# Kernel optimization log

Measured on AMD Instinct MI355X. Metric: run time of the kernel, lower is better.

## Reference

```python
import jax, jax.numpy as jnp
import numpy as np

NUM_USERS = 100000
NUM_ITEMS = 50000
N_NODES = NUM_USERS + NUM_ITEMS
EMB = 64
N_EDGES = 2000000
NUM_LAYERS = 3


def setup_inputs() -> dict:
    key = jax.random.key(0)
    ks = jax.random.split(key, 16)
    inp = {
        "edge_index": jax.random.randint(ks[0], (2, N_EDGES), 0, N_NODES, dtype=jnp.int64 if jax.config.jax_enable_x64 else jnp.int32),
        "user_features": jax.random.normal(ks[1], (NUM_USERS, 15), dtype=jnp.float32),
        "user_color_indices": jax.random.randint(ks[2], (NUM_USERS,), 0, 22),
        "user_size_indices": jax.random.randint(ks[3], (NUM_USERS,), 0, 18),
        "item_features": jax.random.normal(ks[4], (NUM_ITEMS, 17), dtype=jnp.float32),
        "user_emb_w": jax.random.normal(ks[5], (NUM_USERS, EMB), dtype=jnp.float32) * 0.01,
        "item_emb_w": jax.random.normal(ks[6], (NUM_ITEMS, EMB), dtype=jnp.float32) * 0.01,
        "user_numeric_W": jax.random.normal(ks[7], (EMB, 12), dtype=jnp.float32) * 0.1,
        "user_numeric_b": jnp.zeros((EMB,), dtype=jnp.float32),
        "user_vector_W": jax.random.normal(ks[8], (EMB, 3), dtype=jnp.float32) * 0.1,
        "user_vector_b": jnp.zeros((EMB,), dtype=jnp.float32),
        "color_emb_w": jax.random.normal(ks[9], (22, EMB), dtype=jnp.float32) * 0.1,
        "size_emb_w": jax.random.normal(ks[10], (18, EMB), dtype=jnp.float32) * 0.1,
        "item_numeric_W": jax.random.normal(ks[11], (EMB, 5), dtype=jnp.float32) * 0.1,
        "item_numeric_b": jnp.zeros((EMB,), dtype=jnp.float32),
        "item_vector_W": jax.random.normal(ks[12], (EMB, 12), dtype=jnp.float32) * 0.1,
        "item_vector_b": jnp.zeros((EMB,), dtype=jnp.float32),
    }
    return inp


def _lightgcn_conv(x, row, col, norm):
    # gather x at source (row), scale by per-edge norm, scatter-add at target (col)
    msg = norm[:, None] * x[row]                      # [E, d]
    return jax.ops.segment_sum(msg, col, num_segments=N_NODES)


def reference(edge_index, user_features, user_color_indices, user_size_indices,
              item_features, user_emb_w, item_emb_w,
              user_numeric_W, user_numeric_b, user_vector_W, user_vector_b,
              color_emb_w, size_emb_w,
              item_numeric_W, item_numeric_b, item_vector_W, item_vector_b):
    # multimodal feature fusion
    user_emb = (user_emb_w
                + user_features[:, :12] @ user_numeric_W.T + user_numeric_b
                + user_features[:, 12:15] @ user_vector_W.T + user_vector_b
                + color_emb_w[user_color_indices]
                + size_emb_w[user_size_indices])
    item_emb = (item_emb_w
                + item_features[:, :5] @ item_numeric_W.T + item_numeric_b
                + item_features[:, 5:] @ item_vector_W.T + item_vector_b)
    x = jnp.concatenate([user_emb, item_emb], axis=0)  # [N, d]

    row, col = edge_index[0], edge_index[1]
    # symmetric-normalization coefficients (degree over targets, as in source)
    deg = jax.ops.segment_sum(jnp.ones_like(col, dtype=x.dtype), col, num_segments=N_NODES)
    deg_inv_sqrt = jnp.where(deg > 0, jax.lax.rsqrt(jnp.maximum(deg, 1.0)), 0.0)
    norm = deg_inv_sqrt[row] * deg_inv_sqrt[col]       # [E]

    acc = x
    total = x
    for _ in range(NUM_LAYERS):
        acc = _lightgcn_conv(acc, row, col, norm)      # dropout in eval mode = identity
        total = total + acc
    final = total / (NUM_LAYERS + 1)

    return final[:NUM_USERS], final[NUM_USERS:]
```

## Files before the change

### kernel.cpp

```cpp
#include <hip/hip_runtime.h>

#define EMB 64
#define NBMAX 512
#define BCAP 8192
#define BSTRIDE 12288
#define CHUNK 4096


__device__ __forceinline__ unsigned short f2bf(float f) {
    union { float f; unsigned u; } c; c.f = f;
    unsigned r = c.u + 0x7fffu + ((c.u >> 16) & 1u);
    return (unsigned short)(r >> 16);
}
__device__ __forceinline__ float bflo(unsigned u) {
    union { unsigned u; float f; } c; c.u = u << 16; return c.f;
}
__device__ __forceinline__ float bfhi(unsigned u) {
    union { unsigned u; float f; } c; c.u = u & 0xffff0000u; return c.f;
}


__global__ void init_kernel(unsigned* __restrict__ p, int nz,
                            unsigned* __restrict__ dummyA,
                            unsigned* __restrict__ dummyB) {
    int i = blockIdx.x * blockDim.x + threadIdx.x;
    if (i < nz) p[i] = 0u;
    if (blockIdx.x == 0) {
        int t = threadIdx.x;
        if (t < 32) dummyA[t] = 0u;
        else if (t < 64) dummyB[t - 32] = 0u;
    }
}


__global__ void fuse_users_kernel(const float* __restrict__ feat,
                                  const int* __restrict__ cidx,
                                  const int* __restrict__ sidx,
                                  const float* __restrict__ emb_w,
                                  const float* __restrict__ Wn,
                                  const float* __restrict__ bn,
                                  const float* __restrict__ Wv,
                                  const float* __restrict__ bv,
                                  const float* __restrict__ color_w,
                                  const float* __restrict__ size_w,
                                  const float* __restrict__ dis,
                                  float* __restrict__ total,
                                  unsigned short* __restrict__ y0,
                                  int U) {
    int t = blockIdx.x * blockDim.x + threadIdx.x;
    int u = t >> 6, d = t & 63;
    if (u >= U) return;
    const float* f = feat + (size_t)u * 15;
    float acc = emb_w[(size_t)u * EMB + d] + bn[d] + bv[d];
#pragma unroll
    for (int k = 0; k < 12; ++k) acc = fmaf(f[k], Wn[d * 12 + k], acc);
#pragma unroll
    for (int k = 0; k < 3; ++k) acc = fmaf(f[12 + k], Wv[d * 3 + k], acc);
    acc += color_w[(size_t)cidx[u] * EMB + d];
    acc += size_w[(size_t)sidx[u] * EMB + d];
    size_t o = (size_t)u * EMB + d;
    total[o] = acc;
    y0[o] = f2bf(acc * dis[u]);
}

__global__ void fuse_items_kernel(const float* __restrict__ feat,
                                  const float* __restrict__ emb_w,
                                  const float* __restrict__ Wn,
                                  const float* __restrict__ bn,
                                  const float* __restrict__ Wv,
                                  const float* __restrict__ bv,
                                  const float* __restrict__ dis,
                                  float* __restrict__ total,
                                  unsigned short* __restrict__ y0,
                                  int I, int U) {
    int t = blockIdx.x * blockDim.x + threadIdx.x;
    int i = t >> 6, d = t & 63;
    if (i >= I) return;
    const float* f = feat + (size_t)i * 17;
    float acc = emb_w[(size_t)i * EMB + d] + bn[d] + bv[d];
#pragma unroll
    for (int k = 0; k < 5; ++k) acc = fmaf(f[k], Wn[d * 5 + k], acc);
#pragma unroll
    for (int k = 0; k < 12; ++k) acc = fmaf(f[5 + k], Wv[d * 12 + k], acc);
    int n = U + i;
    size_t o = (size_t)n * EMB + d;
    total[o] = acc;
    y0[o] = f2bf(acc * dis[n]);
}


__global__ __launch_bounds__(256) void partition_kernel(
        const int* __restrict__ row, const int* __restrict__ col,
        unsigned* __restrict__ bcursor, unsigned* __restrict__ bucketbuf,
        int E, int NB) {
    __shared__ unsigned h[NBMAX];
    __shared__ unsigned wbase[NBMAX];
    const int t = threadIdx.x;
    const long chunk = (long)blockIdx.x * CHUNK;

    for (int i = t; i < NB; i += 256) h[i] = 0u;
    __syncthreads();
    for (int it = 0; it < CHUNK / 256; ++it) {
        long e = chunk + (long)it * 256 + t;
        if (e < E) atomicAdd(&h[((unsigned)col[e]) >> 9], 1u);
    }
    __syncthreads();
    for (int i = t; i < NB; i += 256) {
        unsigned c = h[i];
        wbase[i] = c ? atomicAdd(&bcursor[i], c) : 0u;
    }
    __syncthreads();
    for (int i = t; i < NB; i += 256) h[i] = 0u;
    __syncthreads();
    for (int it = 0; it < CHUNK / 256; ++it) {
        long e = chunk + (long)it * 256 + t;
        if (e < E) {
            unsigned c = (unsigned)col[e];
            unsigned b = c >> 9;
            unsigned lpos = atomicAdd(&h[b], 1u);
            unsigned pos = wbase[b] + lpos;
            if (pos < BCAP)
                bucketbuf[(size_t)b * BCAP + pos] = (((unsigned)row[e]) << 9) | (c & 511u);
        }
    }
}


__global__ __launch_bounds__(256) void bucket_csr_kernel(
        const unsigned* __restrict__ bcursor,
        const unsigned* __restrict__ bucketbuf,
        uint4* __restrict__ meta,
        float* __restrict__ dis, unsigned* __restrict__ srcidx,
        unsigned* __restrict__ clsCnt,
        int N, int NB) {
    const int b = blockIdx.x;
    const int t = threadIdx.x;
    __shared__ unsigned hist[512];
    __shared__ unsigned ps[256];
    __shared__ unsigned cls[64];

    const unsigned base = (unsigned)b * BSTRIDE;
    unsigned cntb = bcursor[b];
    if (cntb > BCAP) cntb = BCAP;

    hist[2 * t] = 0u; hist[2 * t + 1] = 0u;
    if (t < 64) cls[t] = 0u;
    __syncthreads();
    const unsigned* buf = bucketbuf + (size_t)b * BCAP;
    for (unsigned j = t; j < cntb; j += 256) atomicAdd(&hist[buf[j] & 511u], 1u);
    __syncthreads();

    unsigned h0 = hist[2 * t], h1 = hist[2 * t + 1];
    unsigned c0p = (h0 + 7u) & ~7u, c1p = (h1 + 7u) & ~7u;
    ps[t] = c0p + c1p;
    __syncthreads();
    for (int off = 1; off < 256; off <<= 1) {
        unsigned y = (t >= off) ? ps[t - off] : 0u;
        __syncthreads();
        ps[t] += y;
        __syncthreads();
    }
    unsigned pexcl = ps[t] - (c0p + c1p);
    unsigned beg0 = base + pexcl, beg1 = beg0 + c0p;

    int n0 = (b << 9) + 2 * t, n1 = n0 + 1;
    if (n0 < N) {
        float dv = h0 ? rsqrtf((float)h0) : 0.f;
        meta[n0] = make_uint4(beg0, beg0 + c0p, __float_as_uint(dv), 0u);
        dis[n0] = dv;
        atomicAdd(&cls[min(c0p >> 3, 63u)], 1u);
        for (unsigned k = h0; k < c0p; ++k) srcidx[beg0 + k] = ((unsigned)N) << 5;
    }
    if (n1 < N) {
        float dv = h1 ? rsqrtf((float)h1) : 0.f;
        meta[n1] = make_uint4(beg1, beg1 + c1p, __float_as_uint(dv), 0u);
        dis[n1] = dv;
        atomicAdd(&cls[min(c1p >> 3, 63u)], 1u);
        for (unsigned k = h1; k < c1p; ++k) srcidx[beg1 + k] = ((unsigned)N) << 5;
    }
    __syncthreads();

    if (t < 64 && cls[t]) atomicAdd(&clsCnt[t], cls[t]);
    hist[2 * t] = beg0; hist[2 * t + 1] = beg1;
    __syncthreads();
    for (unsigned j = t; j < cntb; j += 256) {
        unsigned p = buf[j];
        unsigned pos = atomicAdd(&hist[p & 511u], 1u);
        srcidx[pos] = (p >> 9) << 5;
    }
}


__global__ void cls_scan_kernel(const unsigned* __restrict__ clsCnt,
                                unsigned* __restrict__ clsBase) {
    __shared__ unsigned sh[64];
    int t = threadIdx.x;
    if (t < 64) sh[t] = clsCnt[t];
    __syncthreads();
    if (t == 0) {
        unsigned run = 0;
        for (int i = 0; i < 64; ++i) { unsigned v = sh[i]; sh[i] = run; run += v; }
    }
    __syncthreads();
    if (t < 64) clsBase[t] = sh[t];
}


__global__ __launch_bounds__(256) void order_fill_kernel(
        const uint4* __restrict__ meta,
        const unsigned* __restrict__ clsBase, unsigned* __restrict__ clsCur,
        unsigned* __restrict__ order, int N) {
    __shared__ unsigned h[64], wb[64];
    int t = threadIdx.x;
    int n = blockIdx.x * 256 + t;
    if (t < 64) h[t] = 0u;
    __syncthreads();
    unsigned c = 0, lpos = 0;
    bool valid = n < N;
    if (valid) {
        uint4 md = meta[n];
        c = min((md.y - md.x) >> 3, 63u);
        lpos = atomicAdd(&h[c], 1u);
    }
    __syncthreads();
    if (t < 64) wb[t] = h[t] ? atomicAdd(&clsCur[t], h[t]) : 0u;
    __syncthreads();
    if (valid) order[clsBase[c] + wb[c] + lpos] = (unsigned)n;
}


__global__ __launch_bounds__(256) void gather_propagate_kernel(
        const unsigned* __restrict__ order, const uint4* __restrict__ meta,
        const unsigned* __restrict__ src,
        const unsigned* __restrict__ srcidx,
        unsigned* __restrict__ ynext,
        float4* __restrict__ total4,
        float scale, int N, int store) {
    int lane = threadIdx.x & 63;
    int slot = blockIdx.x * 8 + ((threadIdx.x >> 6) << 1) + (lane >> 5);
    bool active = slot < N;
    int n = active ? (int)order[slot] : 0;
    uint4 md = active ? meta[n] : make_uint4(0u, 0u, 0u, 0u);
    unsigned beg = md.x, endp = md.y;
    float dn = __uint_as_float(md.z);
    unsigned q = (unsigned)((lane >> 4) & 1);
    unsigned m2 = (unsigned)(lane & 15) * 2u;
    float s0 = 0.f, s1 = 0.f, s2 = 0.f, s3 = 0.f;
    for (unsigned j = beg; j < endp; j += 8) {
        uint4 iv = *reinterpret_cast<const uint4*>(&srcidx[j + 4u * q]);
        uint2 ua = *reinterpret_cast<const uint2*>(&src[iv.x + m2]);
        uint2 ub = *reinterpret_cast<const uint2*>(&src[iv.y + m2]);
        uint2 uc = *reinterpret_cast<const uint2*>(&src[iv.z + m2]);
        uint2 ud = *reinterpret_cast<const uint2*>(&src[iv.w + m2]);
        s0 += (bflo(ua.x) + bflo(ub.x)) + (bflo(uc.x) + bflo(ud.x));
        s1 += (bfhi(ua.x) + bfhi(ub.x)) + (bfhi(uc.x) + bfhi(ud.x));
        s2 += (bflo(ua.y) + bflo(ub.y)) + (bflo(uc.y) + bflo(ud.y));
        s3 += (bfhi(ua.y) + bfhi(ub.y)) + (bfhi(uc.y) + bfhi(ud.y));
    }
    s0 += __shfl_xor(s0, 16);
    s1 += __shfl_xor(s1, 16);
    s2 += __shfl_xor(s2, 16);
    s3 += __shfl_xor(s3, 16);
    if (active && (lane & 31) < 16) {
        float a0 = dn * s0, a1 = dn * s1, a2 = dn * s2, a3 = dn * s3;
        size_t o4 = (size_t)n * 16 + (m2 >> 1);
        float4 tv = total4[o4];
        total4[o4] = make_float4((tv.x + a0) * scale, (tv.y + a1) * scale,
                                 (tv.z + a2) * scale, (tv.w + a3) * scale);
        if (store) {
            uint2 pk;
            pk.x = (unsigned)f2bf(dn * a0) | ((unsigned)f2bf(dn * a1) << 16);
            pk.y = (unsigned)f2bf(dn * a2) | ((unsigned)f2bf(dn * a3) << 16);
            *reinterpret_cast<uint2*>(&ynext[(size_t)n * 32 + m2]) = pk;
        }
    }
}


extern "C" void kernel_launch(void* const* d_in, const int* in_sizes, int n_in,
                              void* d_out, int out_size, void* d_ws, size_t ws_size,
                              hipStream_t stream) {
    const int*   edge       = (const int*)d_in[0];
    const float* user_feat  = (const float*)d_in[1];
    const int*   cidx       = (const int*)d_in[2];
    const int*   sidx       = (const int*)d_in[3];
    const float* item_feat  = (const float*)d_in[4];
    const float* user_emb_w = (const float*)d_in[5];
    const float* item_emb_w = (const float*)d_in[6];
    const float* uWn        = (const float*)d_in[7];
    const float* ubn        = (const float*)d_in[8];
    const float* uWv        = (const float*)d_in[9];
    const float* ubv        = (const float*)d_in[10];
    const float* color_w    = (const float*)d_in[11];
    const float* size_w     = (const float*)d_in[12];
    const float* iWn        = (const float*)d_in[13];
    const float* ibn        = (const float*)d_in[14];
    const float* iWv        = (const float*)d_in[15];
    const float* ibv        = (const float*)d_in[16];

    const int E = in_sizes[0] / 2;
    const int U = in_sizes[5] / EMB;
    const int I = in_sizes[6] / EMB;
    const int N = U + I;
    const int NB = (N + 511) >> 9;

    const int* row = edge;
    const int* col = edge + E;

    float* total = (float*)d_out;

    unsigned short* yA      = (unsigned short*)d_ws;
    unsigned short* yB      = yA + (size_t)(N + 1) * EMB;
    unsigned*       bucketbuf = (unsigned*)yB;
    unsigned*       srcidx  = (unsigned*)(yB + (size_t)(N + 1) * EMB);
    uint4*          meta    = (uint4*)(srcidx + (size_t)NB * BSTRIDE);
    float*          dis     = (float*)(meta + N);
    unsigned*       bcursor = (unsigned*)(dis + N);
    unsigned*       clsCnt  = bcursor + NB;
    unsigned*       clsCur  = clsCnt + 64;
    unsigned*       clsBase = clsCur + 64;
    unsigned*       order   = clsBase + 64;

    const int TB = 256;

    init_kernel<<<(NB + 128 + TB - 1) / TB, TB, 0, stream>>>(
        bcursor, NB + 128,
        (unsigned*)(yA + (size_t)N * EMB), (unsigned*)(yB + (size_t)N * EMB));
    const int gP = (E + CHUNK - 1) / CHUNK;
    partition_kernel<<<gP, TB, 0, stream>>>(row, col, bcursor, bucketbuf, E, NB);
    bucket_csr_kernel<<<NB, TB, 0, stream>>>(bcursor, bucketbuf, meta, dis,
                                             srcidx, clsCnt, N, NB);
    cls_scan_kernel<<<1, 64, 0, stream>>>(clsCnt, clsBase);
    order_fill_kernel<<<(N + TB - 1) / TB, TB, 0, stream>>>(meta, clsBase,
                                                            clsCur, order, N);

    {
        int gU = (int)(((long)U * EMB + TB - 1) / TB);
        fuse_users_kernel<<<gU, TB, 0, stream>>>(user_feat, cidx, sidx, user_emb_w,
                                                 uWn, ubn, uWv, ubv, color_w, size_w,
                                                 dis, total, yA, U);
        int gI = (int)(((long)I * EMB + TB - 1) / TB);
        fuse_items_kernel<<<gI, TB, 0, stream>>>(item_feat, item_emb_w,
                                                 iWn, ibn, iWv, ibv,
                                                 dis, total, yA, I, U);
    }

    const int gG = (N + 7) / 8;
    gather_propagate_kernel<<<gG, TB, 0, stream>>>(order, meta,
                                                   (const unsigned*)yA, srcidx,
                                                   (unsigned*)yB, (float4*)total,
                                                   1.0f, N, 1);
    gather_propagate_kernel<<<gG, TB, 0, stream>>>(order, meta,
                                                   (const unsigned*)yB, srcidx,
                                                   (unsigned*)yA, (float4*)total,
                                                   1.0f, N, 1);
    gather_propagate_kernel<<<gG, TB, 0, stream>>>(order, meta,
                                                   (const unsigned*)yA, srcidx,
                                                   (unsigned*)yB, (float4*)total,
                                                   0.25f, N, 0);

    (void)n_in; (void)out_size; (void)ws_size;
}
```

Measured before the change: 279.7 us.

## Store running total in bf16, unroll gather loop, widen CSR build blocks

The running sum of layer outputs is kept in a bf16 workspace buffer instead of the fp32 output, with a new finalize kernel that expands it to fp32 and applies the 1/4 scale. This cuts the read-modify-write traffic on the total in each of the three propagation passes, but costs an extra pass and adds rounding error that accumulates over the layers. The gather loop is unrolled to 16 edges per iteration with two accumulator sets to keep more loads in flight. The partition and bucket CSR kernels move to 512-thread blocks with one node per thread.

```diff
diff --git a/kernel.cpp b/kernel.cpp
--- a/kernel.cpp
+++ b/kernel.cpp
@@ -17,6 +17,9 @@
 }
 __device__ __forceinline__ float bfhi(unsigned u) {
     union { unsigned u; float f; } c; c.u = u & 0xffff0000u; return c.f;
+}
+__device__ __forceinline__ unsigned pack2(float a, float b) {
+    return (unsigned)f2bf(a) | ((unsigned)f2bf(b) << 16);
 }
 
 
@@ -44,7 +47,7 @@
                                   const float* __restrict__ color_w,
                                   const float* __restrict__ size_w,
                                   const float* __restrict__ dis,
-                                  float* __restrict__ total,
+                                  unsigned short* __restrict__ totB,
                                   unsigned short* __restrict__ y0,
                                   int U) {
     int t = blockIdx.x * blockDim.x + threadIdx.x;
@@ -59,7 +62,7 @@
     acc += color_w[(size_t)cidx[u] * EMB + d];
     acc += size_w[(size_t)sidx[u] * EMB + d];
     size_t o = (size_t)u * EMB + d;
-    total[o] = acc;
+    totB[o] = f2bf(acc);
     y0[o] = f2bf(acc * dis[u]);
 }
 
@@ -70,7 +73,7 @@
                                   const float* __restrict__ Wv,
                                   const float* __restrict__ bv,
                                   const float* __restrict__ dis,
-                                  float* __restrict__ total,
+                                  unsigned short* __restrict__ totB,
                                   unsigned short* __restrict__ y0,
                                   int I, int U) {
     int t = blockIdx.x * blockDim.x + threadIdx.x;
@@ -84,12 +87,12 @@
     for (int k = 0; k < 12; ++k) acc = fmaf(f[5 + k], Wv[d * 12 + k], acc);
     int n = U + i;
     size_t o = (size_t)n * EMB + d;
-    total[o] = acc;
+    totB[o] = f2bf(acc);
     y0[o] = f2bf(acc * dis[n]);
 }
 
 
-__global__ __launch_bounds__(256) void partition_kernel(
+__global__ __launch_bounds__(512) void partition_kernel(
         const int* __restrict__ row, const int* __restrict__ col,
         unsigned* __restrict__ bcursor, unsigned* __restrict__ bucketbuf,
         int E, int NB) {
@@ -98,22 +101,22 @@
     const int t = threadIdx.x;
     const long chunk = (long)blockIdx.x * CHUNK;
 
-    for (int i = t; i < NB; i += 256) h[i] = 0u;
-    __syncthreads();
-    for (int it = 0; it < CHUNK / 256; ++it) {
-        long e = chunk + (long)it * 256 + t;
+    for (int i = t; i < NB; i += 512) h[i] = 0u;
+    __syncthreads();
+    for (int it = 0; it < CHUNK / 512; ++it) {
+        long e = chunk + (long)it * 512 + t;
         if (e < E) atomicAdd(&h[((unsigned)col[e]) >> 9], 1u);
     }
     __syncthreads();
-    for (int i = t; i < NB; i += 256) {
+    for (int i = t; i < NB; i += 512) {
         unsigned c = h[i];
         wbase[i] = c ? atomicAdd(&bcursor[i], c) : 0u;
     }
     __syncthreads();
-    for (int i = t; i < NB; i += 256) h[i] = 0u;
-    __syncthreads();
-    for (int it = 0; it < CHUNK / 256; ++it) {
-        long e = chunk + (long)it * 256 + t;
+    for (int i = t; i < NB; i += 512) h[i] = 0u;
+    __syncthreads();
+    for (int it = 0; it < CHUNK / 512; ++it) {
+        long e = chunk + (long)it * 512 + t;
         if (e < E) {
             unsigned c = (unsigned)col[e];
             unsigned b = c >> 9;
@@ -126,7 +129,7 @@
 }
 
 
-__global__ __launch_bounds__(256) void bucket_csr_kernel(
+__global__ __launch_bounds__(512) void bucket_csr_kernel(
         const unsigned* __restrict__ bcursor,
         const unsigned* __restrict__ bucketbuf,
         uint4* __restrict__ meta,
@@ -136,34 +139,33 @@
     const int b = blockIdx.x;
     const int t = threadIdx.x;
     __shared__ unsigned hist[512];
-    __shared__ unsigned ps[256];
+    __shared__ unsigned ps[512];
     __shared__ unsigned cls[64];
 
     const unsigned base = (unsigned)b * BSTRIDE;
     unsigned cntb = bcursor[b];
     if (cntb > BCAP) cntb = BCAP;
 
-    hist[2 * t] = 0u; hist[2 * t + 1] = 0u;
+    hist[t] = 0u;
     if (t < 64) cls[t] = 0u;
     __syncthreads();
     const unsigned* buf = bucketbuf + (size_t)b * BCAP;
-    for (unsigned j = t; j < cntb; j += 256) atomicAdd(&hist[buf[j] & 511u], 1u);
-    __syncthreads();
-
-    unsigned h0 = hist[2 * t], h1 = hist[2 * t + 1];
-    unsigned c0p = (h0 + 7u) & ~7u, c1p = (h1 + 7u) & ~7u;
-    ps[t] = c0p + c1p;
-    __syncthreads();
-    for (int off = 1; off < 256; off <<= 1) {
+    for (unsigned j = t; j < cntb; j += 512) atomicAdd(&hist[buf[j] & 511u], 1u);
+    __syncthreads();
+
+    unsigned h0 = hist[t];
+    unsigned c0p = (h0 + 7u) & ~7u;
+    ps[t] = c0p;
+    __syncthreads();
+    for (int off = 1; off < 512; off <<= 1) {
         unsigned y = (t >= off) ? ps[t - off] : 0u;
         __syncthreads();
         ps[t] += y;
         __syncthreads();
     }
-    unsigned pexcl = ps[t] - (c0p + c1p);
-    unsigned beg0 = base + pexcl, beg1 = beg0 + c0p;
-
-    int n0 = (b << 9) + 2 * t, n1 = n0 + 1;
+    unsigned beg0 = base + ps[t] - c0p;
+
+    int n0 = (b << 9) + t;
     if (n0 < N) {
         float dv = h0 ? rsqrtf((float)h0) : 0.f;
         meta[n0] = make_uint4(beg0, beg0 + c0p, __float_as_uint(dv), 0u);
@@ -171,19 +173,12 @@
         atomicAdd(&cls[min(c0p >> 3, 63u)], 1u);
         for (unsigned k = h0; k < c0p; ++k) srcidx[beg0 + k] = ((unsigned)N) << 5;
     }
-    if (n1 < N) {
-        float dv = h1 ? rsqrtf((float)h1) : 0.f;
-        meta[n1] = make_uint4(beg1, beg1 + c1p, __float_as_uint(dv), 0u);
-        dis[n1] = dv;
-        atomicAdd(&cls[min(c1p >> 3, 63u)], 1u);
-        for (unsigned k = h1; k < c1p; ++k) srcidx[beg1 + k] = ((unsigned)N) << 5;
-    }
     __syncthreads();
 
     if (t < 64 && cls[t]) atomicAdd(&clsCnt[t], cls[t]);
-    hist[2 * t] = beg0; hist[2 * t + 1] = beg1;
-    __syncthreads();
-    for (unsigned j = t; j < cntb; j += 256) {
+    hist[t] = beg0;
+    __syncthreads();
+    for (unsigned j = t; j < cntb; j += 512) {
         unsigned p = buf[j];
         unsigned pos = atomicAdd(&hist[p & 511u], 1u);
         srcidx[pos] = (p >> 9) << 5;
@@ -234,8 +229,8 @@
         const unsigned* __restrict__ src,
         const unsigned* __restrict__ srcidx,
         unsigned* __restrict__ ynext,
-        float4* __restrict__ total4,
-        float scale, int N, int store) {
+        unsigned* __restrict__ totB,
+        int N, int store) {
     int lane = threadIdx.x & 63;
     int slot = blockIdx.x * 8 + ((threadIdx.x >> 6) << 1) + (lane >> 5);
     bool active = slot < N;
@@ -246,7 +241,29 @@
     unsigned q = (unsigned)((lane >> 4) & 1);
     unsigned m2 = (unsigned)(lane & 15) * 2u;
     float s0 = 0.f, s1 = 0.f, s2 = 0.f, s3 = 0.f;
-    for (unsigned j = beg; j < endp; j += 8) {
+    float t0 = 0.f, t1 = 0.f, t2 = 0.f, t3 = 0.f;
+    unsigned j = beg;
+    for (; j + 16 <= endp; j += 16) {
+        uint4 iv0 = *reinterpret_cast<const uint4*>(&srcidx[j + 4u * q]);
+        uint4 iv1 = *reinterpret_cast<const uint4*>(&srcidx[j + 8u + 4u * q]);
+        uint2 ua = *reinterpret_cast<const uint2*>(&src[iv0.x + m2]);
+        uint2 ub = *reinterpret_cast<const uint2*>(&src[iv0.y + m2]);
+        uint2 uc = *reinterpret_cast<const uint2*>(&src[iv0.z + m2]);
+        uint2 ud = *reinterpret_cast<const uint2*>(&src[iv0.w + m2]);
+        uint2 ue = *reinterpret_cast<const uint2*>(&src[iv1.x + m2]);
+        uint2 uf = *reinterpret_cast<const uint2*>(&src[iv1.y + m2]);
+        uint2 ug = *reinterpret_cast<const uint2*>(&src[iv1.z + m2]);
+        uint2 uh = *reinterpret_cast<const uint2*>(&src[iv1.w + m2]);
+        s0 += (bflo(ua.x) + bflo(ub.x)) + (bflo(uc.x) + bflo(ud.x));
+        s1 += (bfhi(ua.x) + bfhi(ub.x)) + (bfhi(uc.x) + bfhi(ud.x));
+        s2 += (bflo(ua.y) + bflo(ub.y)) + (bflo(uc.y) + bflo(ud.y));
+        s3 += (bfhi(ua.y) + bfhi(ub.y)) + (bfhi(uc.y) + bfhi(ud.y));
+        t0 += (bflo(ue.x) + bflo(uf.x)) + (bflo(ug.x) + bflo(uh.x));
+        t1 += (bfhi(ue.x) + bfhi(uf.x)) + (bfhi(ug.x) + bfhi(uh.x));
+        t2 += (bflo(ue.y) + bflo(uf.y)) + (bflo(ug.y) + bflo(uh.y));
+        t3 += (bfhi(ue.y) + bfhi(uf.y)) + (bfhi(ug.y) + bfhi(uh.y));
+    }
+    if (j < endp) {
         uint4 iv = *reinterpret_cast<const uint4*>(&srcidx[j + 4u * q]);
         uint2 ua = *reinterpret_cast<const uint2*>(&src[iv.x + m2]);
         uint2 ub = *reinterpret_cast<const uint2*>(&src[iv.y + m2]);
@@ -257,22 +274,35 @@
         s2 += (bflo(ua.y) + bflo(ub.y)) + (bflo(uc.y) + bflo(ud.y));
         s3 += (bfhi(ua.y) + bfhi(ub.y)) + (bfhi(uc.y) + bfhi(ud.y));
     }
+    s0 += t0; s1 += t1; s2 += t2; s3 += t3;
     s0 += __shfl_xor(s0, 16);
     s1 += __shfl_xor(s1, 16);
     s2 += __shfl_xor(s2, 16);
     s3 += __shfl_xor(s3, 16);
     if (active && (lane & 31) < 16) {
         float a0 = dn * s0, a1 = dn * s1, a2 = dn * s2, a3 = dn * s3;
-        size_t o4 = (size_t)n * 16 + (m2 >> 1);
-        float4 tv = total4[o4];
-        total4[o4] = make_float4((tv.x + a0) * scale, (tv.y + a1) * scale,
-                                 (tv.z + a2) * scale, (tv.w + a3) * scale);
+        size_t o = (size_t)n * 32 + m2;
+        uint2 tv = *reinterpret_cast<const uint2*>(&totB[o]);
+        uint2 nv;
+        nv.x = pack2(bflo(tv.x) + a0, bfhi(tv.x) + a1);
+        nv.y = pack2(bflo(tv.y) + a2, bfhi(tv.y) + a3);
+        *reinterpret_cast<uint2*>(&totB[o]) = nv;
         if (store) {
             uint2 pk;
-            pk.x = (unsigned)f2bf(dn * a0) | ((unsigned)f2bf(dn * a1) << 16);
-            pk.y = (unsigned)f2bf(dn * a2) | ((unsigned)f2bf(dn * a3) << 16);
+            pk.x = pack2(dn * a0, dn * a1);
+            pk.y = pack2(dn * a2, dn * a3);
             *reinterpret_cast<uint2*>(&ynext[(size_t)n * 32 + m2]) = pk;
         }
+    }
+}
+
+
+__global__ void finalize_kernel(const unsigned* __restrict__ totB,
+                                float2* __restrict__ out2, long n32) {
+    long t = (long)blockIdx.x * blockDim.x + threadIdx.x;
+    if (t < n32) {
+        unsigned u = totB[t];
+        out2[t] = make_float2(bflo(u) * 0.25f, bfhi(u) * 0.25f);
     }
 }
 
@@ -307,12 +337,11 @@
     const int* row = edge;
     const int* col = edge + E;
 
-    float* total = (float*)d_out;
-
     unsigned short* yA      = (unsigned short*)d_ws;
     unsigned short* yB      = yA + (size_t)(N + 1) * EMB;
     unsigned*       bucketbuf = (unsigned*)yB;
-    unsigned*       srcidx  = (unsigned*)(yB + (size_t)(N + 1) * EMB);
+    unsigned short* totB    = yB + (size_t)(N + 1) * EMB;
+    unsigned*       srcidx  = (unsigned*)(totB + (size_t)N * EMB);
     uint4*          meta    = (uint4*)(srcidx + (size_t)NB * BSTRIDE);
     float*          dis     = (float*)(meta + N);
     unsigned*       bcursor = (unsigned*)(dis + N);
@@ -327,9 +356,9 @@
         bcursor, NB + 128,
         (unsigned*)(yA + (size_t)N * EMB), (unsigned*)(yB + (size_t)N * EMB));
     const int gP = (E + CHUNK - 1) / CHUNK;
-    partition_kernel<<<gP, TB, 0, stream>>>(row, col, bcursor, bucketbuf, E, NB);
-    bucket_csr_kernel<<<NB, TB, 0, stream>>>(bcursor, bucketbuf, meta, dis,
-                                             srcidx, clsCnt, N, NB);
+    partition_kernel<<<gP, 512, 0, stream>>>(row, col, bcursor, bucketbuf, E, NB);
+    bucket_csr_kernel<<<NB, 512, 0, stream>>>(bcursor, bucketbuf, meta, dis,
+                                              srcidx, clsCnt, N, NB);
     cls_scan_kernel<<<1, 64, 0, stream>>>(clsCnt, clsBase);
     order_fill_kernel<<<(N + TB - 1) / TB, TB, 0, stream>>>(meta, clsBase,
                                                             clsCur, order, N);
@@ -338,26 +367,30 @@
         int gU = (int)(((long)U * EMB + TB - 1) / TB);
         fuse_users_kernel<<<gU, TB, 0, stream>>>(user_feat, cidx, sidx, user_emb_w,
                                                  uWn, ubn, uWv, ubv, color_w, size_w,
-                                                 dis, total, yA, U);
+                                                 dis, totB, yA, U);
         int gI = (int)(((long)I * EMB + TB - 1) / TB);
         fuse_items_kernel<<<gI, TB, 0, stream>>>(item_feat, item_emb_w,
                                                  iWn, ibn, iWv, ibv,
-                                                 dis, total, yA, I, U);
+                                                 dis, totB, yA, I, U);
     }
 
     const int gG = (N + 7) / 8;
     gather_propagate_kernel<<<gG, TB, 0, stream>>>(order, meta,
                                                    (const unsigned*)yA, srcidx,
-                                                   (unsigned*)yB, (float4*)total,
-                                                   1.0f, N, 1);
+                                                   (unsigned*)yB, (unsigned*)totB,
+                                                   N, 1);
     gather_propagate_kernel<<<gG, TB, 0, stream>>>(order, meta,
                                                    (const unsigned*)yB, srcidx,
-                                                   (unsigned*)yA, (float4*)total,
-                                                   1.0f, N, 1);
+                                                   (unsigned*)yA, (unsigned*)totB,
+                                                   N, 1);
     gather_propagate_kernel<<<gG, TB, 0, stream>>>(order, meta,
                                                    (const unsigned*)yA, srcidx,
-                                                   (unsigned*)yB, (float4*)total,
-                                                   0.25f, N, 0);
+                                                   (unsigned*)yB, (unsigned*)totB,
+                                                   N, 0);
+
+    const long n32 = (long)N * 32;
+    finalize_kernel<<<(int)((n32 + TB - 1) / TB), TB, 0, stream>>>(
+        (const unsigned*)totB, (float2*)d_out, n32);
 
     (void)n_in; (void)out_size; (void)ws_size;
 }
```

After: 259.2 us. -7.3%, faster.
